# Kernel tuning notes

Hardware: AMD Instinct MI355X
Metric: run time of the kernel (lower is better)

Reference implementation:

```python
import jax, jax.numpy as jnp
import numpy as np

N_NODES = 100000
N_EDGES = 1600000
IN_C = 128
HID = 128
LAT = 64
N_LAYERS = 3
N_GRAPHS = 1000


def setup_inputs() -> dict:
    key = jax.random.key(0)
    ks = jax.random.split(key, 16)
    x = jax.random.normal(ks[0], (N_NODES, IN_C), dtype=jnp.float32)
    edge_index = jax.random.randint(ks[1], (2, N_EDGES), 0, N_NODES, dtype=jnp.int64)
    batch = jnp.sort(jax.random.randint(ks[2], (N_NODES,), 0, N_GRAPHS, dtype=jnp.int64))
    s = 1.0 / np.sqrt(HID)
    # per-layer GIN MLP params (in_c == hidden for all layers since IN_C == HID)
    W1 = jax.random.normal(ks[3], (N_LAYERS, IN_C, HID), dtype=jnp.float32) * s
    b1 = jnp.zeros((N_LAYERS, HID), dtype=jnp.float32)
    W2 = jax.random.normal(ks[4], (N_LAYERS, HID, HID), dtype=jnp.float32) * s
    b2 = jnp.zeros((N_LAYERS, HID), dtype=jnp.float32)
    W_mu = jax.random.normal(ks[5], (HID, LAT), dtype=jnp.float32) * s
    b_mu = jnp.zeros((LAT,), dtype=jnp.float32)
    W_lv = jax.random.normal(ks[6], (HID, LAT), dtype=jnp.float32) * s
    b_lv = jnp.zeros((LAT,), dtype=jnp.float32)
    return {"x": x, "edge_index": edge_index, "batch": batch,
            "W1": W1, "b1": b1, "W2": W2, "b2": b2,
            "W_mu": W_mu, "b_mu": b_mu, "W_lv": W_lv, "b_lv": b_lv}


def reference(x, edge_index, batch, W1, b1, W2, b2, W_mu, b_mu, W_lv, b_lv):
    src, dst = edge_index[0], edge_index[1]
    h = x
    for i in range(N_LAYERS):
        # GINConv (eps=0): h' = MLP(h + sum_{j in N(i)} h_j); scatter-add over edges
        agg = h + jax.ops.segment_sum(h[src], dst, num_segments=N_NODES)
        h = jax.nn.relu(agg @ W1[i] + b1[i])
        h = jax.nn.relu(h @ W2[i] + b2[i])
        h = jax.nn.relu(h)  # extra ReLU in forward after conv (idempotent here)
    # global_add_pool: segment-sum nodes into graphs
    g = jax.ops.segment_sum(h, batch, num_segments=N_GRAPHS)  # [G, HID]
    mu = g @ W_mu + b_mu
    logvar = g @ W_lv + b_lv
    return (mu, logvar)
```

## Files before the change

### kernel.cpp

```cpp
#include <hip/hip_runtime.h>

#define N_NODES 100000
#define N_EDGES 1600000
#define HID 128
#define LAT 64
#define N_LAYERS 3
#define N_GRAPHS 1000
#define CAP 64
#define NBIN 391
#define MAXBIN 4608
#define ACHUNK 8192
#define ABLOCKS ((N_EDGES + ACHUNK - 1) / ACHUNK)
#define CVT_BLOCKS (N_NODES * HID / 4 / 256)

typedef short bf16x8 __attribute__((ext_vector_type(8)));
typedef float f32x4 __attribute__((ext_vector_type(4)));

__device__ __forceinline__ float bf2f(unsigned short h) {
    union { unsigned int u; float f; } c;
    c.u = ((unsigned int)h) << 16;
    return c.f;
}
__device__ __forceinline__ unsigned short f2bf(float f) {
    union { float f; unsigned int u; } c;
    c.f = f;
    unsigned int u = c.u;
    return (unsigned short)((u + 0x7fffu + ((u >> 16) & 1u)) >> 16);
}
__device__ __forceinline__ unsigned int pack2(float a, float b) {
    return (unsigned int)f2bf(a) | ((unsigned int)f2bf(b) << 16);
}
__device__ __forceinline__ void addrow(float* acc, uint4 w) {
    acc[0] += bf2f((unsigned short)w.x); acc[1] += bf2f((unsigned short)(w.x >> 16));
    acc[2] += bf2f((unsigned short)w.y); acc[3] += bf2f((unsigned short)(w.y >> 16));
    acc[4] += bf2f((unsigned short)w.z); acc[5] += bf2f((unsigned short)(w.z >> 16));
    acc[6] += bf2f((unsigned short)w.w); acc[7] += bf2f((unsigned short)(w.w >> 16));
}

__global__ __launch_bounds__(256) void setup_kernel(const int* __restrict__ ei,
                                                    int* __restrict__ gcnt,
                                                    unsigned int* __restrict__ ebin,
                                                    const float* __restrict__ x,
                                                    unsigned short* __restrict__ xb,
                                                    const float* __restrict__ W1,
                                                    const float* __restrict__ W2,
                                                    unsigned short* __restrict__ Wt) {
    __shared__ unsigned int scount[NBIN];
    __shared__ unsigned int sfill[NBIN];
    int t = threadIdx.x;
    int blk = blockIdx.x;
    if (blk >= ABLOCKS) {
        int b2 = blk - ABLOCKS;
        if (b2 < 6) {
            const float* W = ((b2 & 1) ? W2 : W1) + (size_t)(b2 >> 1) * HID * HID;
            unsigned short* D = Wt + (size_t)b2 * HID * HID;
            for (int idx = t; idx < HID * HID; idx += 256) {
                int n = idx >> 7, k = idx & 127;
                D[n * HID + k] = f2bf(W[k * HID + n]);
            }
            return;
        }
        int i = (b2 - 6) * 256 + t;
        if (i >= N_NODES * HID / 4) return;
        float4 v = ((const float4*)x)[i];
        ((uint2*)xb)[i] = make_uint2(pack2(v.x, v.y), pack2(v.z, v.w));
        return;
    }
    int base = blk * ACHUNK;
    int n = N_EDGES - base;
    if (n > ACHUNK) n = ACHUNK;
    for (int i = t; i < NBIN; i += 256) scount[i] = 0u;
    __syncthreads();
    for (int i = t; i < n; i += 256) {
        int d = ei[N_EDGES + base + i];
        atomicAdd(&scount[d >> 8], 1u);
    }
    __syncthreads();
    for (int b = t; b < NBIN; b += 256) {
        unsigned int c = scount[b];
        sfill[b] = c ? (unsigned int)atomicAdd(&gcnt[b], (int)c) : 0u;
    }
    __syncthreads();
    for (int i = t; i < n; i += 256) {
        int s = ei[base + i];
        int d = ei[N_EDGES + base + i];
        int b = d >> 8;
        unsigned int pos = atomicAdd(&sfill[b], 1u);
        ebin[(size_t)b * MAXBIN + pos] = ((unsigned int)(d & 255) << 24) | (unsigned int)s;
    }
}

__global__ __launch_bounds__(256) void binB_kernel(const unsigned int* __restrict__ ebin,
                                                   const int* __restrict__ gcnt,
                                                   int* __restrict__ cnt,
                                                   int* __restrict__ csr) {
    __shared__ int scnt[256];
    int b = blockIdx.x;
    int t = threadIdx.x;
    scnt[t] = 0;
    __syncthreads();
    int n0 = b << 8;
    int c = gcnt[b];
    const unsigned int* src = ebin + (size_t)b * MAXBIN;
    for (int i = t; i < c; i += 256) {
        unsigned int e = src[i];
        int dl = (int)(e >> 24);
        int slot = atomicAdd(&scnt[dl], 1);
        csr[(size_t)(n0 + dl) * CAP + slot] = (int)(e & 0xFFFFFFu);
    }
    __syncthreads();
    int node = n0 + t;
    if (node < N_NODES) cnt[node] = scnt[t];
}

__global__ __launch_bounds__(256) void fused_kernel(const unsigned short* __restrict__ h,
                                                    const int* __restrict__ cnt,
                                                    const int* __restrict__ csr,
                                                    const unsigned short* __restrict__ W1t,
                                                    const float* __restrict__ b1,
                                                    const unsigned short* __restrict__ W2t,
                                                    const float* __restrict__ b2,
                                                    unsigned short* __restrict__ out,
                                                    const int* __restrict__ batch,
                                                    float* __restrict__ gpool) {
    __shared__ unsigned short sA[16][136];
    __shared__ int sbatch[16];
    const int t = threadIdx.x;
    const int w = t >> 6;
    const int l = t & 63;
    const int lm = l & 15;
    const int quad = l >> 4;
    const int row0 = blockIdx.x * 16;

    if (gpool && t < 16) {
        int n = row0 + t;
        sbatch[t] = (n < N_NODES) ? batch[n] : -1;
    }

    {
        const int q = t & 15;
        const int rloc = t >> 4;
        int node = row0 + rloc;
        float acc[8] = {0.f, 0.f, 0.f, 0.f, 0.f, 0.f, 0.f, 0.f};
        if (node < N_NODES) {
            addrow(acc, *(const uint4*)(h + (size_t)node * HID + q * 8));
            const int* nl = csr + (size_t)node * CAP;
            int deg = cnt[node];
            int e = 0;
            for (; e + 8 <= deg; e += 8) {
                int s0 = nl[e], s1 = nl[e + 1], s2 = nl[e + 2], s3 = nl[e + 3];
                int s4 = nl[e + 4], s5 = nl[e + 5], s6 = nl[e + 6], s7 = nl[e + 7];
                uint4 w0 = *(const uint4*)(h + (size_t)s0 * HID + q * 8);
                uint4 w1 = *(const uint4*)(h + (size_t)s1 * HID + q * 8);
                uint4 w2 = *(const uint4*)(h + (size_t)s2 * HID + q * 8);
                uint4 w3 = *(const uint4*)(h + (size_t)s3 * HID + q * 8);
                uint4 w4 = *(const uint4*)(h + (size_t)s4 * HID + q * 8);
                uint4 w5 = *(const uint4*)(h + (size_t)s5 * HID + q * 8);
                uint4 w6 = *(const uint4*)(h + (size_t)s6 * HID + q * 8);
                uint4 w7 = *(const uint4*)(h + (size_t)s7 * HID + q * 8);
                addrow(acc, w0); addrow(acc, w1); addrow(acc, w2); addrow(acc, w3);
                addrow(acc, w4); addrow(acc, w5); addrow(acc, w6); addrow(acc, w7);
            }
            for (; e + 4 <= deg; e += 4) {
                int s0 = nl[e], s1 = nl[e + 1], s2 = nl[e + 2], s3 = nl[e + 3];
                uint4 w0 = *(const uint4*)(h + (size_t)s0 * HID + q * 8);
                uint4 w1 = *(const uint4*)(h + (size_t)s1 * HID + q * 8);
                uint4 w2 = *(const uint4*)(h + (size_t)s2 * HID + q * 8);
                uint4 w3 = *(const uint4*)(h + (size_t)s3 * HID + q * 8);
                addrow(acc, w0); addrow(acc, w1); addrow(acc, w2); addrow(acc, w3);
            }
            for (; e < deg; ++e) {
                addrow(acc, *(const uint4*)(h + (size_t)nl[e] * HID + q * 8));
            }
        }
        uint4 o;
        o.x = pack2(acc[0], acc[1]);
        o.y = pack2(acc[2], acc[3]);
        o.z = pack2(acc[4], acc[5]);
        o.w = pack2(acc[6], acc[7]);
        *(uint4*)&sA[rloc][q * 8] = o;
    }
    __syncthreads();

    const unsigned short* Wt2[2] = {W1t, W2t};
    const float* bias[2] = {b1, b2};
    const int n0a = (2 * w) * 16 + lm;
    const int n0b = (2 * w + 1) * 16 + lm;

    for (int p = 0; p < 2; ++p) {
        f32x4 acc0 = (f32x4){0.f, 0.f, 0.f, 0.f};
        f32x4 acc1 = (f32x4){0.f, 0.f, 0.f, 0.f};
        const unsigned short* Wp = Wt2[p];
#pragma unroll
        for (int kc = 0; kc < 4; ++kc) {
            bf16x8 a = *(const bf16x8*)&sA[lm][kc * 32 + quad * 8];
            bf16x8 bfr0 = *(const bf16x8*)(Wp + (size_t)n0a * HID + kc * 32 + quad * 8);
            bf16x8 bfr1 = *(const bf16x8*)(Wp + (size_t)n0b * HID + kc * 32 + quad * 8);
            acc0 = __builtin_amdgcn_mfma_f32_16x16x32_bf16(a, bfr0, acc0, 0, 0, 0);
            acc1 = __builtin_amdgcn_mfma_f32_16x16x32_bf16(a, bfr1, acc1, 0, 0, 0);
        }
        __syncthreads();
        float bv0 = bias[p][n0a];
        float bv1 = bias[p][n0b];
#pragma unroll
        for (int r = 0; r < 4; ++r) {
            int m = quad * 4 + r;
            sA[m][n0a] = f2bf(fmaxf(acc0[r] + bv0, 0.f));
            sA[m][n0b] = f2bf(fmaxf(acc1[r] + bv1, 0.f));
        }
        __syncthreads();
    }

    if (!gpool) {
        int r = t >> 4, c = t & 15;
        int grow = row0 + r;
        if (grow < N_NODES)
            *(uint4*)(out + (size_t)grow * HID + c * 8) = *(const uint4*)&sA[r][c * 8];
    } else {
        int c = t & 127;
        int r0 = (t >> 7) * 8;
        float acc = 0.f;
        int cur = sbatch[r0];
        for (int r = r0; r < r0 + 8; ++r) {
            int b = sbatch[r];
            if (b < 0) break;
            if (b != cur) {
                atomicAdd(&gpool[(size_t)cur * HID + c], acc);
                acc = 0.f;
                cur = b;
            }
            acc += bf2f(sA[r][c]);
        }
        if (cur >= 0) atomicAdd(&gpool[(size_t)cur * HID + c], acc);
    }
}

__global__ __launch_bounds__(128) void head_kernel(const float* __restrict__ g,
                                                   const float* __restrict__ Wmu,
                                                   const float* __restrict__ bmu,
                                                   const float* __restrict__ Wlv,
                                                   const float* __restrict__ blv,
                                                   float* __restrict__ out) {
    __shared__ float sg[HID];
    int gi = blockIdx.x;
    sg[threadIdx.x] = g[(size_t)gi * HID + threadIdx.x];
    __syncthreads();
    int j = threadIdx.x & 63;
    bool is_lv = threadIdx.x >= 64;
    const float* W = is_lv ? Wlv : Wmu;
    float acc = is_lv ? blv[j] : bmu[j];
    for (int k = 0; k < HID; ++k) acc = fmaf(sg[k], W[k * LAT + j], acc);
    out[(is_lv ? (size_t)N_GRAPHS * LAT : 0) + (size_t)gi * LAT + j] = acc;
}

extern "C" void kernel_launch(void* const* d_in, const int* in_sizes, int n_in,
                              void* d_out, int out_size, void* d_ws, size_t ws_size,
                              hipStream_t stream) {
    const float* x     = (const float*)d_in[0];
    const int*   ei    = (const int*)d_in[1];
    const int*   batch = (const int*)d_in[2];
    const float* W1    = (const float*)d_in[3];
    const float* b1    = (const float*)d_in[4];
    const float* W2    = (const float*)d_in[5];
    const float* b2    = (const float*)d_in[6];
    const float* Wmu   = (const float*)d_in[7];
    const float* bmu   = (const float*)d_in[8];
    const float* Wlv   = (const float*)d_in[9];
    const float* blv   = (const float*)d_in[10];
    float* out = (float*)d_out;

    unsigned short* xb   = (unsigned short*)d_ws;
    unsigned short* h1   = xb + (size_t)N_NODES * HID;
    unsigned short* h2   = h1 + (size_t)N_NODES * HID;
    int* csr = (int*)(h2 + (size_t)N_NODES * HID);
    unsigned int* ebin = (unsigned int*)(csr + (size_t)N_NODES * CAP);
    unsigned short* Wt = (unsigned short*)(ebin + (size_t)NBIN * MAXBIN);
    float* g  = (float*)(Wt + (size_t)6 * HID * HID);
    int* gcnt = (int*)(g + (size_t)N_GRAPHS * HID);
    int* cnt  = gcnt + NBIN + 1;

    hipMemsetAsync(g, 0, (size_t)N_GRAPHS * HID * sizeof(float) + (NBIN + 1) * sizeof(int),
                   stream);

    setup_kernel<<<ABLOCKS + 6 + CVT_BLOCKS, 256, 0, stream>>>(ei, gcnt, ebin,
                                                               x, xb, W1, W2, Wt);
    binB_kernel<<<NBIN, 256, 0, stream>>>(ebin, gcnt, cnt, csr);

    const unsigned short* hcur = xb;
    unsigned short* hdst = h1;
    for (int i = 0; i < N_LAYERS; ++i) {
        bool last = (i == N_LAYERS - 1);
        fused_kernel<<<(N_NODES + 15) / 16, 256, 0, stream>>>(
            hcur, cnt, csr,
            Wt + (size_t)(2 * i) * HID * HID, b1 + (size_t)i * HID,
            Wt + (size_t)(2 * i + 1) * HID * HID, b2 + (size_t)i * HID,
            hdst, batch, last ? g : nullptr);
        hcur = hdst;
        hdst = (hdst == h1) ? h2 : h1;
    }
    head_kernel<<<N_GRAPHS, 128, 0, stream>>>(g, Wmu, bmu, Wlv, blv, out);
}
```

Baseline: 428.8 us.

## Give each wave its own 16-row tile to remove block-wide barriers

Each block now handles 64 nodes, and each of its four waves owns a private 16-row shared-memory tile. Every wave does its own neighbor aggregation, both MLP GEMMs over all 128 output columns (8 MFMA accumulators), and the writeback or pooling. This removes all __syncthreads calls and cuts the block count by a factor of four. In exchange, each wave loads the full weight matrix (more global and L2 weight traffic per node), uses more registers for accumulators, and each wave does the gather over four row-iterations serially.

```diff
diff --git a/kernel.cpp b/kernel.cpp
--- a/kernel.cpp
+++ b/kernel.cpp
@@ -123,23 +123,23 @@
                                                     unsigned short* __restrict__ out,
                                                     const int* __restrict__ batch,
                                                     float* __restrict__ gpool) {
-    __shared__ unsigned short sA[16][136];
-    __shared__ int sbatch[16];
+    __shared__ unsigned short sA[4][16][136];
+    __shared__ int sbatch[4][16];
     const int t = threadIdx.x;
     const int w = t >> 6;
     const int l = t & 63;
     const int lm = l & 15;
     const int quad = l >> 4;
-    const int row0 = blockIdx.x * 16;
-
-    if (gpool && t < 16) {
-        int n = row0 + t;
-        sbatch[t] = (n < N_NODES) ? batch[n] : -1;
-    }
-
-    {
-        const int q = t & 15;
-        const int rloc = t >> 4;
+    const int row0 = blockIdx.x * 64 + w * 16;
+
+    if (gpool && l < 16) {
+        int n = row0 + l;
+        sbatch[w][l] = (n < N_NODES) ? batch[n] : -1;
+    }
+
+    const int q = lm;
+    for (int it = 0; it < 4; ++it) {
+        int rloc = it * 4 + quad;
         int node = row0 + rloc;
         float acc[8] = {0.f, 0.f, 0.f, 0.f, 0.f, 0.f, 0.f, 0.f};
         if (node < N_NODES) {
@@ -178,60 +178,64 @@
         o.y = pack2(acc[2], acc[3]);
         o.z = pack2(acc[4], acc[5]);
         o.w = pack2(acc[6], acc[7]);
-        *(uint4*)&sA[rloc][q * 8] = o;
-    }
-    __syncthreads();
+        *(uint4*)&sA[w][rloc][q * 8] = o;
+    }
 
     const unsigned short* Wt2[2] = {W1t, W2t};
     const float* bias[2] = {b1, b2};
-    const int n0a = (2 * w) * 16 + lm;
-    const int n0b = (2 * w + 1) * 16 + lm;
 
     for (int p = 0; p < 2; ++p) {
-        f32x4 acc0 = (f32x4){0.f, 0.f, 0.f, 0.f};
-        f32x4 acc1 = (f32x4){0.f, 0.f, 0.f, 0.f};
+        f32x4 acc[8];
+#pragma unroll
+        for (int nt = 0; nt < 8; ++nt) acc[nt] = (f32x4){0.f, 0.f, 0.f, 0.f};
         const unsigned short* Wp = Wt2[p];
 #pragma unroll
         for (int kc = 0; kc < 4; ++kc) {
-            bf16x8 a = *(const bf16x8*)&sA[lm][kc * 32 + quad * 8];
-            bf16x8 bfr0 = *(const bf16x8*)(Wp + (size_t)n0a * HID + kc * 32 + quad * 8);
-            bf16x8 bfr1 = *(const bf16x8*)(Wp + (size_t)n0b * HID + kc * 32 + quad * 8);
-            acc0 = __builtin_amdgcn_mfma_f32_16x16x32_bf16(a, bfr0, acc0, 0, 0, 0);
-            acc1 = __builtin_amdgcn_mfma_f32_16x16x32_bf16(a, bfr1, acc1, 0, 0, 0);
-        }
-        __syncthreads();
-        float bv0 = bias[p][n0a];
-        float bv1 = bias[p][n0b];
-#pragma unroll
-        for (int r = 0; r < 4; ++r) {
-            int m = quad * 4 + r;
-            sA[m][n0a] = f2bf(fmaxf(acc0[r] + bv0, 0.f));
-            sA[m][n0b] = f2bf(fmaxf(acc1[r] + bv1, 0.f));
-        }
-        __syncthreads();
+            bf16x8 a = *(const bf16x8*)&sA[w][lm][kc * 32 + quad * 8];
+#pragma unroll
+            for (int nt = 0; nt < 8; ++nt) {
+                bf16x8 b = *(const bf16x8*)(Wp + (size_t)(nt * 16 + lm) * HID
+                                               + kc * 32 + quad * 8);
+                acc[nt] = __builtin_amdgcn_mfma_f32_16x16x32_bf16(a, b, acc[nt], 0, 0, 0);
+            }
+        }
+#pragma unroll
+        for (int nt = 0; nt < 8; ++nt) {
+            float bv = bias[p][nt * 16 + lm];
+#pragma unroll
+            for (int r = 0; r < 4; ++r) {
+                sA[w][quad * 4 + r][nt * 16 + lm] = f2bf(fmaxf(acc[nt][r] + bv, 0.f));
+            }
+        }
     }
 
     if (!gpool) {
-        int r = t >> 4, c = t & 15;
-        int grow = row0 + r;
-        if (grow < N_NODES)
-            *(uint4*)(out + (size_t)grow * HID + c * 8) = *(const uint4*)&sA[r][c * 8];
+#pragma unroll
+        for (int i = 0; i < 4; ++i) {
+            int idx = i * 64 + l;
+            int r = idx >> 4, c = idx & 15;
+            int grow = row0 + r;
+            if (grow < N_NODES)
+                *(uint4*)(out + (size_t)grow * HID + c * 8) = *(const uint4*)&sA[w][r][c * 8];
+        }
     } else {
-        int c = t & 127;
-        int r0 = (t >> 7) * 8;
-        float acc = 0.f;
-        int cur = sbatch[r0];
-        for (int r = r0; r < r0 + 8; ++r) {
-            int b = sbatch[r];
-            if (b < 0) break;
-            if (b != cur) {
-                atomicAdd(&gpool[(size_t)cur * HID + c], acc);
-                acc = 0.f;
-                cur = b;
-            }
-            acc += bf2f(sA[r][c]);
-        }
-        if (cur >= 0) atomicAdd(&gpool[(size_t)cur * HID + c], acc);
+#pragma unroll
+        for (int half = 0; half < 2; ++half) {
+            int c = half * 64 + l;
+            float acc = 0.f;
+            int cur = sbatch[w][0];
+            for (int r = 0; r < 16; ++r) {
+                int b = sbatch[w][r];
+                if (b < 0) break;
+                if (b != cur) {
+                    atomicAdd(&gpool[(size_t)cur * HID + c], acc);
+                    acc = 0.f;
+                    cur = b;
+                }
+                acc += bf2f(sA[w][r][c]);
+            }
+            if (cur >= 0) atomicAdd(&gpool[(size_t)cur * HID + c], acc);
+        }
     }
 }
 
@@ -290,7 +294,7 @@
     unsigned short* hdst = h1;
     for (int i = 0; i < N_LAYERS; ++i) {
         bool last = (i == N_LAYERS - 1);
-        fused_kernel<<<(N_NODES + 15) / 16, 256, 0, stream>>>(
+        fused_kernel<<<(N_NODES + 63) / 64, 256, 0, stream>>>(
             hcur, cnt, csr,
             Wt + (size_t)(2 * i) * HID * HID, b1 + (size_t)i * HID,
             Wt + (size_t)(2 * i + 1) * HID * HID, b2 + (size_t)i * HID,
```

Result: slower. 473.4 us (+10.4%).

## Split fused gather+MLP kernel into separate gather and MLP kernels

Applied to the files above, without the earlier changes.

Unfuses the per-layer kernel into a neighbor-gather kernel that writes the aggregated features to a bf16 buffer, and an MLP kernel that reads that buffer and runs the two MFMA matmuls. The gather kernel runs with 512-thread blocks so it can keep more memory-latency-bound gathers in flight, free of the MLP's register and LDS pressure. The cost is one extra write and read of a 100000x128 bf16 buffer per layer plus an extra launch. Output double buffering is replaced by a single hbuf, which is safe because gather reads hbuf only before mlp2 overwrites it.

```diff
diff --git a/kernel.cpp b/kernel.cpp
--- a/kernel.cpp
+++ b/kernel.cpp
@@ -113,16 +113,60 @@
     if (node < N_NODES) cnt[node] = scnt[t];
 }
 
-__global__ __launch_bounds__(256) void fused_kernel(const unsigned short* __restrict__ h,
-                                                    const int* __restrict__ cnt,
-                                                    const int* __restrict__ csr,
-                                                    const unsigned short* __restrict__ W1t,
-                                                    const float* __restrict__ b1,
-                                                    const unsigned short* __restrict__ W2t,
-                                                    const float* __restrict__ b2,
-                                                    unsigned short* __restrict__ out,
-                                                    const int* __restrict__ batch,
-                                                    float* __restrict__ gpool) {
+__global__ __launch_bounds__(512) void gather_kernel(const unsigned short* __restrict__ h,
+                                                     const int* __restrict__ cnt,
+                                                     const int* __restrict__ csr,
+                                                     unsigned short* __restrict__ agg) {
+    int t = threadIdx.x;
+    int node = blockIdx.x * 32 + (t >> 4);
+    int q = t & 15;
+    if (node >= N_NODES) return;
+    const int* nl = csr + (size_t)node * CAP;
+    int deg = cnt[node];
+    float acc[8] = {0.f, 0.f, 0.f, 0.f, 0.f, 0.f, 0.f, 0.f};
+    addrow(acc, *(const uint4*)(h + (size_t)node * HID + q * 8));
+    int e = 0;
+    for (; e + 8 <= deg; e += 8) {
+        int s0 = nl[e], s1 = nl[e + 1], s2 = nl[e + 2], s3 = nl[e + 3];
+        int s4 = nl[e + 4], s5 = nl[e + 5], s6 = nl[e + 6], s7 = nl[e + 7];
+        uint4 w0 = *(const uint4*)(h + (size_t)s0 * HID + q * 8);
+        uint4 w1 = *(const uint4*)(h + (size_t)s1 * HID + q * 8);
+        uint4 w2 = *(const uint4*)(h + (size_t)s2 * HID + q * 8);
+        uint4 w3 = *(const uint4*)(h + (size_t)s3 * HID + q * 8);
+        uint4 w4 = *(const uint4*)(h + (size_t)s4 * HID + q * 8);
+        uint4 w5 = *(const uint4*)(h + (size_t)s5 * HID + q * 8);
+        uint4 w6 = *(const uint4*)(h + (size_t)s6 * HID + q * 8);
+        uint4 w7 = *(const uint4*)(h + (size_t)s7 * HID + q * 8);
+        addrow(acc, w0); addrow(acc, w1); addrow(acc, w2); addrow(acc, w3);
+        addrow(acc, w4); addrow(acc, w5); addrow(acc, w6); addrow(acc, w7);
+    }
+    for (; e + 4 <= deg; e += 4) {
+        int s0 = nl[e], s1 = nl[e + 1], s2 = nl[e + 2], s3 = nl[e + 3];
+        uint4 w0 = *(const uint4*)(h + (size_t)s0 * HID + q * 8);
+        uint4 w1 = *(const uint4*)(h + (size_t)s1 * HID + q * 8);
+        uint4 w2 = *(const uint4*)(h + (size_t)s2 * HID + q * 8);
+        uint4 w3 = *(const uint4*)(h + (size_t)s3 * HID + q * 8);
+        addrow(acc, w0); addrow(acc, w1); addrow(acc, w2); addrow(acc, w3);
+    }
+    for (; e < deg; ++e) {
+        addrow(acc, *(const uint4*)(h + (size_t)nl[e] * HID + q * 8));
+    }
+    uint4 o;
+    o.x = pack2(acc[0], acc[1]);
+    o.y = pack2(acc[2], acc[3]);
+    o.z = pack2(acc[4], acc[5]);
+    o.w = pack2(acc[6], acc[7]);
+    *(uint4*)(agg + (size_t)node * HID + q * 8) = o;
+}
+
+__global__ __launch_bounds__(256) void mlp2_kernel(const unsigned short* __restrict__ A,
+                                                   const unsigned short* __restrict__ W1t,
+                                                   const float* __restrict__ b1,
+                                                   const unsigned short* __restrict__ W2t,
+                                                   const float* __restrict__ b2,
+                                                   unsigned short* __restrict__ out,
+                                                   const int* __restrict__ batch,
+                                                   float* __restrict__ gpool) {
     __shared__ unsigned short sA[16][136];
     __shared__ int sbatch[16];
     const int t = threadIdx.x;
@@ -132,60 +176,23 @@
     const int quad = l >> 4;
     const int row0 = blockIdx.x * 16;
 
+    {
+        int r = t >> 4, c = t & 15;
+        int grow = row0 + r;
+        uint4 v = make_uint4(0u, 0u, 0u, 0u);
+        if (grow < N_NODES) v = *(const uint4*)(A + (size_t)grow * HID + c * 8);
+        *(uint4*)&sA[r][c * 8] = v;
+    }
     if (gpool && t < 16) {
         int n = row0 + t;
         sbatch[t] = (n < N_NODES) ? batch[n] : -1;
     }
-
-    {
-        const int q = t & 15;
-        const int rloc = t >> 4;
-        int node = row0 + rloc;
-        float acc[8] = {0.f, 0.f, 0.f, 0.f, 0.f, 0.f, 0.f, 0.f};
-        if (node < N_NODES) {
-            addrow(acc, *(const uint4*)(h + (size_t)node * HID + q * 8));
-            const int* nl = csr + (size_t)node * CAP;
-            int deg = cnt[node];
-            int e = 0;
-            for (; e + 8 <= deg; e += 8) {
-                int s0 = nl[e], s1 = nl[e + 1], s2 = nl[e + 2], s3 = nl[e + 3];
-                int s4 = nl[e + 4], s5 = nl[e + 5], s6 = nl[e + 6], s7 = nl[e + 7];
-                uint4 w0 = *(const uint4*)(h + (size_t)s0 * HID + q * 8);
-                uint4 w1 = *(const uint4*)(h + (size_t)s1 * HID + q * 8);
-                uint4 w2 = *(const uint4*)(h + (size_t)s2 * HID + q * 8);
-                uint4 w3 = *(const uint4*)(h + (size_t)s3 * HID + q * 8);
-                uint4 w4 = *(const uint4*)(h + (size_t)s4 * HID + q * 8);
-                uint4 w5 = *(const uint4*)(h + (size_t)s5 * HID + q * 8);
-                uint4 w6 = *(const uint4*)(h + (size_t)s6 * HID + q * 8);
-                uint4 w7 = *(const uint4*)(h + (size_t)s7 * HID + q * 8);
-                addrow(acc, w0); addrow(acc, w1); addrow(acc, w2); addrow(acc, w3);
-                addrow(acc, w4); addrow(acc, w5); addrow(acc, w6); addrow(acc, w7);
-            }
-            for (; e + 4 <= deg; e += 4) {
-                int s0 = nl[e], s1 = nl[e + 1], s2 = nl[e + 2], s3 = nl[e + 3];
-                uint4 w0 = *(const uint4*)(h + (size_t)s0 * HID + q * 8);
-                uint4 w1 = *(const uint4*)(h + (size_t)s1 * HID + q * 8);
-                uint4 w2 = *(const uint4*)(h + (size_t)s2 * HID + q * 8);
-                uint4 w3 = *(const uint4*)(h + (size_t)s3 * HID + q * 8);
-                addrow(acc, w0); addrow(acc, w1); addrow(acc, w2); addrow(acc, w3);
-            }
-            for (; e < deg; ++e) {
-                addrow(acc, *(const uint4*)(h + (size_t)nl[e] * HID + q * 8));
-            }
-        }
-        uint4 o;
-        o.x = pack2(acc[0], acc[1]);
-        o.y = pack2(acc[2], acc[3]);
-        o.z = pack2(acc[4], acc[5]);
-        o.w = pack2(acc[6], acc[7]);
-        *(uint4*)&sA[rloc][q * 8] = o;
-    }
-    __syncthreads();
-
+    __syncthreads();
+
+    const int n0a = (2 * w) * 16 + lm;
+    const int n0b = (2 * w + 1) * 16 + lm;
     const unsigned short* Wt2[2] = {W1t, W2t};
     const float* bias[2] = {b1, b2};
-    const int n0a = (2 * w) * 16 + lm;
-    const int n0b = (2 * w + 1) * 16 + lm;
 
     for (int p = 0; p < 2; ++p) {
         f32x4 acc0 = (f32x4){0.f, 0.f, 0.f, 0.f};
@@ -270,9 +277,9 @@
     float* out = (float*)d_out;
 
     unsigned short* xb   = (unsigned short*)d_ws;
-    unsigned short* h1   = xb + (size_t)N_NODES * HID;
-    unsigned short* h2   = h1 + (size_t)N_NODES * HID;
-    int* csr = (int*)(h2 + (size_t)N_NODES * HID);
+    unsigned short* agg  = xb + (size_t)N_NODES * HID;
+    unsigned short* hbuf = agg + (size_t)N_NODES * HID;
+    int* csr = (int*)(hbuf + (size_t)N_NODES * HID);
     unsigned int* ebin = (unsigned int*)(csr + (size_t)N_NODES * CAP);
     unsigned short* Wt = (unsigned short*)(ebin + (size_t)NBIN * MAXBIN);
     float* g  = (float*)(Wt + (size_t)6 * HID * HID);
@@ -287,16 +294,14 @@
     binB_kernel<<<NBIN, 256, 0, stream>>>(ebin, gcnt, cnt, csr);
 
     const unsigned short* hcur = xb;
-    unsigned short* hdst = h1;
     for (int i = 0; i < N_LAYERS; ++i) {
         bool last = (i == N_LAYERS - 1);
-        fused_kernel<<<(N_NODES + 15) / 16, 256, 0, stream>>>(
-            hcur, cnt, csr,
-            Wt + (size_t)(2 * i) * HID * HID, b1 + (size_t)i * HID,
-            Wt + (size_t)(2 * i + 1) * HID * HID, b2 + (size_t)i * HID,
-            hdst, batch, last ? g : nullptr);
-        hcur = hdst;
-        hdst = (hdst == h1) ? h2 : h1;
+        gather_kernel<<<(N_NODES + 31) / 32, 512, 0, stream>>>(hcur, cnt, csr, agg);
+        mlp2_kernel<<<(N_NODES + 15) / 16, 256, 0, stream>>>(
+            agg, Wt + (size_t)(2 * i) * HID * HID, b1 + (size_t)i * HID,
+            Wt + (size_t)(2 * i + 1) * HID * HID, b2 + (size_t)i * HID, hbuf,
+            batch, last ? g : nullptr);
+        hcur = hbuf;
     }
     head_kernel<<<N_GRAPHS, 128, 0, stream>>>(g, Wmu, bmu, Wlv, blv, out);
 }
```

Measured after the change: 496.8 us. +15.9%, slower.
